# Kernel optimization log

Measured on AMD Instinct MI355X. Metric: run time of the kernel, lower is better.

The kernel has to match this reference:

```python
import jax, jax.numpy as jnp
import numpy as np

N = 50000      # nodes
E = 640000     # edges (before self loops)
IN = 128       # in_channels
H = 4          # heads (layer 1)
C = 64         # hidden_channels per head
OUT = 64       # out_channels
SLOPE = 0.2    # PyG GATConv default negative_slope


def setup_inputs() -> dict:
    key = jax.random.key(0)
    ks = jax.random.split(key, 12)
    x = jax.random.normal(ks[0], (N, IN), dtype=jnp.float32)
    edge_src = jax.random.randint(ks[1], (E,), 0, N, dtype=jnp.int32)
    edge_dst = jax.random.randint(ks[2], (E,), 0, N, dtype=jnp.int32)
    # Layer 1 params: Linear IN -> H*C, attention vectors a_src/a_dst [H, C], bias [H*C]
    W1 = jax.random.normal(ks[3], (IN, H * C), dtype=jnp.float32) / np.sqrt(IN)
    att_src1 = jax.random.normal(ks[4], (H, C), dtype=jnp.float32) / np.sqrt(C)
    att_dst1 = jax.random.normal(ks[5], (H, C), dtype=jnp.float32) / np.sqrt(C)
    b1 = jnp.zeros((H * C,), dtype=jnp.float32)
    # Layer 2 params: Linear H*C -> OUT, 1 head
    W2 = jax.random.normal(ks[6], (H * C, OUT), dtype=jnp.float32) / np.sqrt(H * C)
    att_src2 = jax.random.normal(ks[7], (1, OUT), dtype=jnp.float32) / np.sqrt(OUT)
    att_dst2 = jax.random.normal(ks[8], (1, OUT), dtype=jnp.float32) / np.sqrt(OUT)
    b2 = jnp.zeros((OUT,), dtype=jnp.float32)
    return {"x": x, "W1": W1, "att_src1": att_src1, "att_dst1": att_dst1, "b1": b1,
            "W2": W2, "att_src2": att_src2, "att_dst2": att_dst2, "b2": b2,
            "edge_src": edge_src, "edge_dst": edge_dst}


def gat_conv(x, src, dst, W, a_src, a_dst, b, heads, ch):
    """PyG GATConv (concat=True): gather -> LeakyReLU attention -> per-dst softmax -> scatter-add."""
    n = x.shape[0]
    h = (x @ W).reshape(n, heads, ch)                  # [N, H, C]
    al_s = jnp.sum(h * a_src, axis=-1)                 # [N, H] node-level src attention term
    al_d = jnp.sum(h * a_dst, axis=-1)                 # [N, H]
    e = jax.nn.leaky_relu(al_s[src] + al_d[dst], SLOPE)  # [E, H] edge scores
    m = jax.ops.segment_max(e, dst, num_segments=n)    # stable per-dst softmax
    ex = jnp.exp(e - m[dst])
    den = jax.ops.segment_sum(ex, dst, num_segments=n)
    alpha = ex / den[dst]                              # [E, H]
    msg = h[src] * alpha[:, :, None]                   # [E, H, C]
    out = jax.ops.segment_sum(msg, dst, num_segments=n)  # [N, H, C]
    return out.reshape(n, heads * ch) + b


def reference(x, W1, att_src1, att_dst1, b1, W2, att_src2, att_dst2, b2, edge_src, edge_dst):
    # PyG GATConv default add_self_loops=True
    loops = jnp.arange(N, dtype=edge_src.dtype)
    src = jnp.concatenate([edge_src, loops])
    dst = jnp.concatenate([edge_dst, loops])
    h = gat_conv(x, src, dst, W1, att_src1, att_dst1, b1, H, C)
    h = jax.nn.elu(h)                                  # F.elu; dropout p=0 -> no-op
    out = gat_conv(h, src, dst, W2, att_src2, att_dst2, b2, 1, OUT)
    return out
```

## Files before the change

kernel.cpp:

```cpp
#include <hip/hip_runtime.h>
#include <hip/hip_bf16.h>
#include <cstdint>
#include <cstddef>

#define N_NODES 50000
#define N_EDGES 640000
#define ET (N_EDGES + N_NODES)
#define IN_CH 128
#define H1 4
#define HC1 256
#define OUT_CH 64
#define SLOPE 0.2f
#define SCAN_NBLK ((N_NODES + 255) / 256)
#define XW (N_NODES * IN_CH / 8)
#define W1N (IN_CH * HC1)
#define W2N (HC1 * OUT_CH)
#define CONVB ((XW + W1N + W2N + 255) / 256)
#define EDGEB ((ET + 255) / 256)
#define MT ((N_NODES + 63) / 64)
#define G1B (4 * MT)
#define PADB SCAN_NBLK
#define DUMMY N_NODES

typedef __attribute__((ext_vector_type(8))) short short8;
typedef __attribute__((ext_vector_type(4))) float floatx4;

__device__ __forceinline__ float bf2f(unsigned short u) {
    return __uint_as_float(((unsigned)u) << 16);
}
__device__ __forceinline__ unsigned short f2bf(float f) {
    unsigned u = __float_as_uint(f);
    unsigned r = 0x7fffu + ((u >> 16) & 1u);
    return (unsigned short)((u + r) >> 16);
}
__device__ __forceinline__ float ldf(const void* p, size_t i, bool f32) {
    return f32 ? ((const float*)p)[i] : bf2f(((const unsigned short*)p)[i]);
}
#define BLO(u) __uint_as_float((u) << 16)
#define BHI(u) __uint_as_float((u) & 0xffff0000u)

__global__ __launch_bounds__(256) void init_all(
    const unsigned short* __restrict__ x, unsigned* __restrict__ flag,
    int* __restrict__ counts, int* __restrict__ state,
    unsigned short* __restrict__ h16, unsigned short* __restrict__ h2,
    float* __restrict__ als1, float* __restrict__ als2)
{
    int b = blockIdx.x;
    if (b < SCAN_NBLK) {
        int i = b * 256 + threadIdx.x;
        if (i < N_NODES) counts[i] = 0;
    } else {
        int t = threadIdx.x;
        if (t < 64) {
            int bad = 0;
            #pragma unroll
            for (int r = 0; r < 4; ++r) {
                float v = bf2f(x[r * 64 + t]);
                if (!(v == v) || fabsf(v) > 1e4f) bad = 1;
            }
            unsigned long long m = __ballot(bad != 0);
            if (t == 0) *flag = (m != 0ull) ? 1u : 0u;
        } else if (t == 64) {
            state[0] = 0; state[1] = 0;
        } else if (t >= 128 && t < 192) {
            uint2 z; z.x = 0u; z.y = 0u;
            *((uint2*)(h16 + (size_t)DUMMY * HC1) + (t - 128)) = z;
        } else if (t >= 192 && t < 224) {
            ((unsigned*)(h2 + (size_t)DUMMY * OUT_CH))[t - 192] = 0u;
        } else if (t >= 224 && t < 228) {
            als1[(size_t)DUMMY * H1 + (t - 224)] = -1e30f;
        } else if (t == 228) {
            als2[DUMMY] = -1e30f;
        }
    }
}

__global__ __launch_bounds__(256) void conv_count(
    const void* __restrict__ x, const void* __restrict__ W1,
    const void* __restrict__ W2, const unsigned* __restrict__ flag,
    unsigned short* __restrict__ x16,
    unsigned short* __restrict__ Wt1, unsigned short* __restrict__ Wt2,
    const int* __restrict__ edst, int* __restrict__ counts,
    int* __restrict__ epos)
{
    int b = blockIdx.x;
    if (b < CONVB) {
        int i = b * 256 + threadIdx.x;
        const bool f32 = (*flag != 0);
        if (i < XW) {
            size_t off = (size_t)i * 8;
            uint4 st;
            if (f32) {
                const float* xp = (const float*)x + off;
                float4 a = *(const float4*)xp;
                float4 c = *(const float4*)(xp + 4);
                st.x = (unsigned)f2bf(a.x) | ((unsigned)f2bf(a.y) << 16);
                st.y = (unsigned)f2bf(a.z) | ((unsigned)f2bf(a.w) << 16);
                st.z = (unsigned)f2bf(c.x) | ((unsigned)f2bf(c.y) << 16);
                st.w = (unsigned)f2bf(c.z) | ((unsigned)f2bf(c.w) << 16);
            } else {
                st = *(const uint4*)((const unsigned short*)x + off);
            }
            *(uint4*)(x16 + off) = st;
        } else if (i < XW + W1N) {
            int j = i - XW;
            int n = j / IN_CH, k = j % IN_CH;
            Wt1[j] = f2bf(ldf(W1, (size_t)k * HC1 + n, f32));
        } else if (i < XW + W1N + W2N) {
            int j = i - XW - W1N;
            int n = j / HC1, k = j % HC1;
            Wt2[j] = f2bf(ldf(W2, (size_t)k * OUT_CH + n, f32));
        }
    } else {
        int i = (b - CONVB) * 256 + threadIdx.x;
        if (i < ET) {
            int d = (i < N_EDGES) ? edst[i] : (i - N_EDGES);
            epos[i] = atomicAdd(&counts[d], 1);
        }
    }
}

__global__ __launch_bounds__(256) void scan_onepass(
    const int* __restrict__ counts, int* __restrict__ rowptr,
    int* __restrict__ bsum, int* __restrict__ boff, int* __restrict__ state)
{
    __shared__ int s[256];
    const int t = threadIdx.x, b = blockIdx.x;
    const int i = b * 256 + t;
    int v = (i < N_NODES) ? ((counts[i] + 7) & ~7) : 0;
    s[t] = v;
    __syncthreads();
    #pragma unroll
    for (int off = 1; off < 256; off <<= 1) {
        int u = (t >= off) ? s[t - off] : 0;
        __syncthreads();
        s[t] += u;
        __syncthreads();
    }
    const int incl = s[t];
    if (t == 255) {
        __hip_atomic_store(&bsum[b], incl, __ATOMIC_RELAXED, __HIP_MEMORY_SCOPE_AGENT);
        __hip_atomic_fetch_add(&state[0], 1, __ATOMIC_ACQ_REL, __HIP_MEMORY_SCOPE_AGENT);
    }
    if (b == 0) {
        if (t == 0) {
            while (__hip_atomic_load(&state[0], __ATOMIC_ACQUIRE, __HIP_MEMORY_SCOPE_AGENT) < SCAN_NBLK)
                __builtin_amdgcn_s_sleep(8);
        }
        __syncthreads();
        int w = (t < SCAN_NBLK)
              ? __hip_atomic_load(&bsum[t], __ATOMIC_RELAXED, __HIP_MEMORY_SCOPE_AGENT) : 0;
        s[t] = w;
        __syncthreads();
        #pragma unroll
        for (int off = 1; off < 256; off <<= 1) {
            int u = (t >= off) ? s[t - off] : 0;
            __syncthreads();
            s[t] += u;
            __syncthreads();
        }
        if (t < SCAN_NBLK)
            __hip_atomic_store(&boff[t], s[t] - w, __ATOMIC_RELAXED, __HIP_MEMORY_SCOPE_AGENT);
        __syncthreads();
        if (t == 0)
            __hip_atomic_store(&state[1], 1, __ATOMIC_RELEASE, __HIP_MEMORY_SCOPE_AGENT);
    }
    if (t == 0) {
        while (__hip_atomic_load(&state[1], __ATOMIC_ACQUIRE, __HIP_MEMORY_SCOPE_AGENT) == 0)
            __builtin_amdgcn_s_sleep(8);
    }
    __syncthreads();
    int off0 = __hip_atomic_load(&boff[b], __ATOMIC_RELAXED, __HIP_MEMORY_SCOPE_AGENT);
    if (i < N_NODES)
        rowptr[i] = off0 + incl - v;
    if (i == N_NODES - 1) rowptr[N_NODES] = off0 + incl;
}

template <int KK, int NSUB>
__device__ __forceinline__ void gemm_body(
    const unsigned short* __restrict__ A, const unsigned short* __restrict__ Bt,
    const void* __restrict__ avs, const void* __restrict__ avd,
    const unsigned* __restrict__ flag, unsigned short* __restrict__ C,
    float* __restrict__ als, float* __restrict__ ald,
    int M, int N, int bx, int by)
{
    const int tid = threadIdx.x;
    const int m0 = by * 64, n0 = bx * (NSUB * 16);
    const int w = tid >> 6, lane = tid & 63;
    const int ln = lane & 15, quad = lane >> 4;
    const int m_frag = m0 + w * 16 + ln;
    floatx4 acc[NSUB];
    #pragma unroll
    for (int sub = 0; sub < NSUB; ++sub)
        acc[sub] = (floatx4){0.f, 0.f, 0.f, 0.f};

    for (int ks = 0; ks < KK / 32; ++ks) {
        const int kbase = ks * 32 + quad * 8;
        short8 a;
        if (m_frag < M) {
            a = *(const short8*)(A + (size_t)m_frag * KK + kbase);
        } else {
            #pragma unroll
            for (int j = 0; j < 8; ++j) a[j] = 0;
        }
        #pragma unroll
        for (int sub = 0; sub < NSUB; ++sub) {
            short8 b = *(const short8*)(Bt + (size_t)(n0 + sub * 16 + ln) * KK + kbase);
            acc[sub] = __builtin_amdgcn_mfma_f32_16x16x32_bf16(a, b, acc[sub], 0, 0, 0);
        }
    }

    #pragma unroll
    for (int sub = 0; sub < NSUB; ++sub) {
        #pragma unroll
        for (int r = 0; r < 4; ++r) {
            int m = m0 + w * 16 + quad * 4 + r;
            if (m < M)
                C[(size_t)m * N + n0 + sub * 16 + ln] = f2bf(acc[sub][r]);
        }
    }

    const bool f32in = (*flag != 0);
    float as[NSUB], av[NSUB];
    #pragma unroll
    for (int sub = 0; sub < NSUB; ++sub) {
        as[sub] = ldf(avs, n0 + sub * 16 + ln, f32in);
        av[sub] = ldf(avd, n0 + sub * 16 + ln, f32in);
    }
    const int Hh = N >> 6;
    #pragma unroll
    for (int hb = 0; hb < NSUB / 4; ++hb) {
        #pragma unroll
        for (int r = 0; r < 4; ++r) {
            float ps = 0.f, pd = 0.f;
            #pragma unroll
            for (int k = 0; k < 4; ++k) {
                ps += acc[hb * 4 + k][r] * as[hb * 4 + k];
                pd += acc[hb * 4 + k][r] * av[hb * 4 + k];
            }
            #pragma unroll
            for (int off = 1; off < 16; off <<= 1) {
                ps += __shfl_xor(ps, off, 64);
                pd += __shfl_xor(pd, off, 64);
            }
            int m = m0 + w * 16 + quad * 4 + r;
            if (ln == 0 && m < M) {
                als[(size_t)m * Hh + bx * (NSUB / 4) + hb] = ps;
                ald[(size_t)m * Hh + bx * (NSUB / 4) + hb] = pd;
            }
        }
    }
}

__global__ __launch_bounds__(256) void gemm1_fill(
    const unsigned short* __restrict__ x16, const unsigned short* __restrict__ Wt1,
    const void* __restrict__ as1, const void* __restrict__ ad1,
    const unsigned* __restrict__ flag, unsigned short* __restrict__ h16,
    float* __restrict__ als, float* __restrict__ ald,
    const int* __restrict__ esrc, const int* __restrict__ edst,
    const int* __restrict__ rowptr, const int* __restrict__ epos,
    const int* __restrict__ counts, int* __restrict__ ecsr)
{
    int b = blockIdx.x;
    if (b < G1B) {
        gemm_body<IN_CH, 4>(x16, Wt1, as1, ad1, flag, h16, als, ald,
                            N_NODES, HC1, b & 3, b >> 2);
    } else if (b < G1B + EDGEB) {
        int i = (b - G1B) * 256 + threadIdx.x;
        if (i < ET) {
            int s = (i < N_EDGES) ? esrc[i] : (i - N_EDGES);
            int d = (i < N_EDGES) ? edst[i] : (i - N_EDGES);
            ecsr[rowptr[d] + epos[i]] = s;
        }
    } else {
        int i = (b - G1B - EDGEB) * 256 + threadIdx.x;
        if (i < N_NODES) {
            int c = counts[i];
            int lo = rowptr[i] + c, hi = rowptr[i + 1];
            for (int j = lo; j < hi; ++j) ecsr[j] = DUMMY;
        }
    }
}

__global__ __launch_bounds__(256) void gemm2(
    const unsigned short* __restrict__ xo16, const unsigned short* __restrict__ Wt2,
    const void* __restrict__ as2, const void* __restrict__ ad2,
    const unsigned* __restrict__ flag, unsigned short* __restrict__ h2,
    float* __restrict__ als, float* __restrict__ ald)
{
    gemm_body<HC1, 4>(xo16, Wt2, as2, ad2, flag, h2, als, ald,
                      N_NODES, OUT_CH, 0, blockIdx.x);
}

__global__ __launch_bounds__(256) void agg_node1(
    const int* __restrict__ rowptr, const int* __restrict__ ecsr,
    const unsigned short* __restrict__ h, const float* __restrict__ als,
    const float* __restrict__ ald, const void* __restrict__ bias,
    const unsigned* __restrict__ flag, unsigned short* __restrict__ out)
{
    int wave = (blockIdx.x * blockDim.x + threadIdx.x) >> 6;
    int lane = threadIdx.x & 63;
    if (wave >= N_NODES) return;
    const int d = wave;
    const int g  = lane >> 5;
    const int hg = (lane >> 3) & 3;
    const int c0 = (lane & 7) << 3;
    const int hoff = hg * 64 + c0;
    const int lo = rowptr[d], hi = rowptr[d + 1];
    const float ad = ald[d * H1 + hg];

    float acc[8];
    #pragma unroll
    for (int j = 0; j < 8; ++j) acc[j] = 0.f;
    float den = 0.f;

    for (int e = lo; e < hi; e += 4) {
        int4 ix = *(const int4*)(ecsr + e);
        int s0 = g ? ix.y : ix.x;
        int s1 = g ? ix.w : ix.z;
        uint4 qa = *(const uint4*)(h + (size_t)s0 * HC1 + hoff);
        uint4 qb = *(const uint4*)(h + (size_t)s1 * HC1 + hoff);
        float t0 = als[s0 * H1 + hg] + ad;
        float t1 = als[s1 * H1 + hg] + ad;
        float p0 = __expf(fmaxf(t0, SLOPE * t0));
        float p1 = __expf(fmaxf(t1, SLOPE * t1));
        den += p0 + p1;
        acc[0] += p0 * BLO(qa.x) + p1 * BLO(qb.x);
        acc[1] += p0 * BHI(qa.x) + p1 * BHI(qb.x);
        acc[2] += p0 * BLO(qa.y) + p1 * BLO(qb.y);
        acc[3] += p0 * BHI(qa.y) + p1 * BHI(qb.y);
        acc[4] += p0 * BLO(qa.z) + p1 * BLO(qb.z);
        acc[5] += p0 * BHI(qa.z) + p1 * BHI(qb.z);
        acc[6] += p0 * BLO(qa.w) + p1 * BLO(qb.w);
        acc[7] += p0 * BHI(qa.w) + p1 * BHI(qb.w);
    }

    den += __shfl_xor(den, 32, 64);
    #pragma unroll
    for (int j = 0; j < 8; ++j) acc[j] += __shfl_xor(acc[j], 32, 64);

    if (lane < 32) {
        const bool f32in = (*flag != 0);
        const float inv = 1.f / den;
        float v[8];
        #pragma unroll
        for (int j = 0; j < 8; ++j) {
            float t = acc[j] * inv + ldf(bias, hoff + j, f32in);
            v[j] = (t > 0.f) ? t : (__expf(t) - 1.f);
        }
        uint4 st;
        st.x = (unsigned)f2bf(v[0]) | ((unsigned)f2bf(v[1]) << 16);
        st.y = (unsigned)f2bf(v[2]) | ((unsigned)f2bf(v[3]) << 16);
        st.z = (unsigned)f2bf(v[4]) | ((unsigned)f2bf(v[5]) << 16);
        st.w = (unsigned)f2bf(v[6]) | ((unsigned)f2bf(v[7]) << 16);
        *(uint4*)(out + (size_t)d * HC1 + hoff) = st;
    }
}

__global__ __launch_bounds__(256) void agg_node2(
    const int* __restrict__ rowptr, const int* __restrict__ ecsr,
    const unsigned short* __restrict__ h, const float* __restrict__ als,
    const float* __restrict__ ald, const void* __restrict__ bias,
    const unsigned* __restrict__ flag, float* __restrict__ out)
{
    int wave = (blockIdx.x * blockDim.x + threadIdx.x) >> 6;
    int lane = threadIdx.x & 63;
    if (wave >= N_NODES) return;
    const int d = wave;
    const int eg = lane >> 3;
    const int c0 = (lane & 7) << 3;
    const int lo = rowptr[d], hi = rowptr[d + 1];
    const float ad = ald[d];

    float acc[8];
    #pragma unroll
    for (int j = 0; j < 8; ++j) acc[j] = 0.f;
    float den = 0.f;

    for (int eb = lo; eb < hi; eb += 8) {
        int s = ecsr[eb + eg];
        uint4 q = *(const uint4*)(h + (size_t)s * OUT_CH + c0);
        float t = als[s] + ad;
        float p = __expf(fmaxf(t, SLOPE * t));
        den += p;
        acc[0] += p * BLO(q.x);
        acc[1] += p * BHI(q.x);
        acc[2] += p * BLO(q.y);
        acc[3] += p * BHI(q.y);
        acc[4] += p * BLO(q.z);
        acc[5] += p * BHI(q.z);
        acc[6] += p * BLO(q.w);
        acc[7] += p * BHI(q.w);
    }
    #pragma unroll
    for (int off = 8; off <= 32; off <<= 1) {
        den += __shfl_xor(den, off, 64);
        #pragma unroll
        for (int j = 0; j < 8; ++j) acc[j] += __shfl_xor(acc[j], off, 64);
    }
    if (lane < 8) {
        const bool f32in = (*flag != 0);
        const float inv = 1.f / den;
        float4 v0, v1;
        v0.x = acc[0] * inv + ldf(bias, c0 + 0, f32in);
        v0.y = acc[1] * inv + ldf(bias, c0 + 1, f32in);
        v0.z = acc[2] * inv + ldf(bias, c0 + 2, f32in);
        v0.w = acc[3] * inv + ldf(bias, c0 + 3, f32in);
        v1.x = acc[4] * inv + ldf(bias, c0 + 4, f32in);
        v1.y = acc[5] * inv + ldf(bias, c0 + 5, f32in);
        v1.z = acc[6] * inv + ldf(bias, c0 + 6, f32in);
        v1.w = acc[7] * inv + ldf(bias, c0 + 7, f32in);
        *(float4*)(out + (size_t)d * OUT_CH + c0) = v0;
        *(float4*)(out + (size_t)d * OUT_CH + c0 + 4) = v1;
    }
}

extern "C" void kernel_launch(void* const* d_in, const int* in_sizes, int n_in,
                              void* d_out, int out_size, void* d_ws, size_t ws_size,
                              hipStream_t stream)
{
    const void* x   = d_in[0];
    const void* W1  = d_in[1];
    const void* as1 = d_in[2];
    const void* ad1 = d_in[3];
    const void* b1  = d_in[4];
    const void* W2  = d_in[5];
    const void* as2 = d_in[6];
    const void* ad2 = d_in[7];
    const void* b2  = d_in[8];
    const int* esrc = (const int*)d_in[9];
    const int* edst = (const int*)d_in[10];
    float* out = (float*)d_out;

    char* base = (char*)d_ws;
    const size_t MB = 1024 * 1024;
    unsigned short* x16  = (unsigned short*)(base);
    unsigned short* h16  = (unsigned short*)(base + 13 * MB);
    unsigned short* xo16 = (unsigned short*)(base + 39 * MB);
    unsigned short* h2   = (unsigned short*)(base + 65 * MB);
    float* als1   = (float*)(base + 72 * MB);
    float* ald1   = (float*)(base + 73 * MB);
    float* als2   = (float*)(base + 74 * MB);
    float* ald2   = (float*)(base + 74 * MB + 512 * 1024);
    unsigned short* Wt1 = (unsigned short*)(base + 75 * MB);
    unsigned short* Wt2 = (unsigned short*)(base + 75 * MB + 128 * 1024);
    int* counts   = (int*)(base + 76 * MB);
    int* rowptr   = (int*)(base + 77 * MB);
    int* bsum     = (int*)(base + 78 * MB);
    int* boff     = bsum + 256;
    int* state    = boff + 256;
    unsigned* flag = (unsigned*)(base + 78 * MB + 8 * 1024);
    int* epos     = (int*)(base + 79 * MB);
    int* ecsr     = (int*)(base + 82 * MB);

    const int BLK = 256;
    const int node_wave_blocks = (N_NODES * 64 + BLK - 1) / BLK;

    init_all<<<SCAN_NBLK + 1, BLK, 0, stream>>>(
        (const unsigned short*)x, flag, counts, state, h16, h2, als1, als2);

    conv_count<<<CONVB + EDGEB, BLK, 0, stream>>>(
        x, W1, W2, flag, x16, Wt1, Wt2, edst, counts, epos);

    scan_onepass<<<SCAN_NBLK, BLK, 0, stream>>>(
        counts, rowptr, bsum, boff, state);

    gemm1_fill<<<G1B + EDGEB + PADB, BLK, 0, stream>>>(
        x16, Wt1, as1, ad1, flag, h16, als1, ald1, esrc, edst, rowptr, epos,
        counts, ecsr);

    agg_node1<<<node_wave_blocks, BLK, 0, stream>>>(
        rowptr, ecsr, h16, als1, ald1, b1, flag, xo16);

    gemm2<<<MT, BLK, 0, stream>>>(xo16, Wt2, as2, ad2, flag, h2, als2, ald2);

    agg_node2<<<node_wave_blocks, BLK, 0, stream>>>(
        rowptr, ecsr, h2, als2, ald2, b2, flag, out);
}
```

Baseline: 291.5 us.

## Drop CSR row padding and mask tail edges in aggregation loops

Removes the per-node padding of CSR rows to multiples of 8, so the DUMMY fill blocks disappear and no padded edges are processed. Both aggregation kernels now handle partial tails with clamped loads and DUMMY-masked sources. Layer-1 aggregation is restructured so each lane loads one edge index and computes one attention exponential per (edge, head), then broadcasts sources and weights with shuffles, processing 16 edges per iteration. This cuts redundant exp and index work but adds many cross-lane shuffles and serialised gathers inside the inner loop.

Result: no change. 290.5 us (-0.4%).

```diff
diff --git a/kernel.cpp b/kernel.cpp
--- a/kernel.cpp
+++ b/kernel.cpp
@@ -19,7 +19,6 @@
 #define EDGEB ((ET + 255) / 256)
 #define MT ((N_NODES + 63) / 64)
 #define G1B (4 * MT)
-#define PADB SCAN_NBLK
 #define DUMMY N_NODES
 
 typedef __attribute__((ext_vector_type(8))) short short8;
@@ -127,7 +126,7 @@
     __shared__ int s[256];
     const int t = threadIdx.x, b = blockIdx.x;
     const int i = b * 256 + t;
-    int v = (i < N_NODES) ? ((counts[i] + 7) & ~7) : 0;
+    int v = (i < N_NODES) ? counts[i] : 0;
     s[t] = v;
     __syncthreads();
     #pragma unroll
@@ -259,25 +258,18 @@
     float* __restrict__ als, float* __restrict__ ald,
     const int* __restrict__ esrc, const int* __restrict__ edst,
     const int* __restrict__ rowptr, const int* __restrict__ epos,
-    const int* __restrict__ counts, int* __restrict__ ecsr)
+    int* __restrict__ ecsr)
 {
     int b = blockIdx.x;
     if (b < G1B) {
         gemm_body<IN_CH, 4>(x16, Wt1, as1, ad1, flag, h16, als, ald,
                             N_NODES, HC1, b & 3, b >> 2);
-    } else if (b < G1B + EDGEB) {
+    } else {
         int i = (b - G1B) * 256 + threadIdx.x;
         if (i < ET) {
             int s = (i < N_EDGES) ? esrc[i] : (i - N_EDGES);
             int d = (i < N_EDGES) ? edst[i] : (i - N_EDGES);
             ecsr[rowptr[d] + epos[i]] = s;
-        }
-    } else {
-        int i = (b - G1B - EDGEB) * 256 + threadIdx.x;
-        if (i < N_NODES) {
-            int c = counts[i];
-            int lo = rowptr[i] + c, hi = rowptr[i + 1];
-            for (int j = lo; j < hi; ++j) ecsr[j] = DUMMY;
         }
     }
 }
@@ -306,36 +298,43 @@
     const int hg = (lane >> 3) & 3;
     const int c0 = (lane & 7) << 3;
     const int hoff = hg * 64 + c0;
+    const int el = lane & 15;
+    const int eo = lane >> 2;
+    const int ho = lane & 3;
     const int lo = rowptr[d], hi = rowptr[d + 1];
-    const float ad = ald[d * H1 + hg];
+    const float adv = ald[d * H1 + ho];
 
     float acc[8];
     #pragma unroll
     for (int j = 0; j < 8; ++j) acc[j] = 0.f;
     float den = 0.f;
 
-    for (int e = lo; e < hi; e += 4) {
-        int4 ix = *(const int4*)(ecsr + e);
-        int s0 = g ? ix.y : ix.x;
-        int s1 = g ? ix.w : ix.z;
-        uint4 qa = *(const uint4*)(h + (size_t)s0 * HC1 + hoff);
-        uint4 qb = *(const uint4*)(h + (size_t)s1 * HC1 + hoff);
-        float t0 = als[s0 * H1 + hg] + ad;
-        float t1 = als[s1 * H1 + hg] + ad;
-        float p0 = __expf(fmaxf(t0, SLOPE * t0));
-        float p1 = __expf(fmaxf(t1, SLOPE * t1));
-        den += p0 + p1;
-        acc[0] += p0 * BLO(qa.x) + p1 * BLO(qb.x);
-        acc[1] += p0 * BHI(qa.x) + p1 * BHI(qb.x);
-        acc[2] += p0 * BLO(qa.y) + p1 * BLO(qb.y);
-        acc[3] += p0 * BHI(qa.y) + p1 * BHI(qb.y);
-        acc[4] += p0 * BLO(qa.z) + p1 * BLO(qb.z);
-        acc[5] += p0 * BHI(qa.z) + p1 * BHI(qb.z);
-        acc[6] += p0 * BLO(qa.w) + p1 * BLO(qb.w);
-        acc[7] += p0 * BHI(qa.w) + p1 * BHI(qb.w);
-    }
-
-    den += __shfl_xor(den, 32, 64);
+    for (int base = lo; base < hi; base += 16) {
+        int ep = base + el;
+        int sv = ecsr[min(ep, hi - 1)];
+        sv = (ep < hi) ? sv : DUMMY;
+        int s_own = __shfl(sv, eo, 64);
+        float t = als[s_own * H1 + ho] + adv;
+        float pv = __expf(fmaxf(t, SLOPE * t));
+        den += pv;
+        #pragma unroll
+        for (int j = 0; j < 8; ++j) {
+            int e2 = 2 * j + g;
+            int s  = __shfl(sv, e2, 64);
+            float p = __shfl(pv, e2 * 4 + hg, 64);
+            uint4 q = *(const uint4*)(h + (size_t)s * HC1 + hoff);
+            acc[0] += p * BLO(q.x); acc[1] += p * BHI(q.x);
+            acc[2] += p * BLO(q.y); acc[3] += p * BHI(q.y);
+            acc[4] += p * BLO(q.z); acc[5] += p * BHI(q.z);
+            acc[6] += p * BLO(q.w); acc[7] += p * BHI(q.w);
+        }
+    }
+
+    #pragma unroll
+    for (int off = 4; off <= 32; off <<= 1)
+        den += __shfl_xor(den, off, 64);
+    den = __shfl(den, hg, 64);
+
     #pragma unroll
     for (int j = 0; j < 8; ++j) acc[j] += __shfl_xor(acc[j], 32, 64);
 
@@ -377,20 +376,25 @@
     for (int j = 0; j < 8; ++j) acc[j] = 0.f;
     float den = 0.f;
 
-    for (int eb = lo; eb < hi; eb += 8) {
-        int s = ecsr[eb + eg];
-        uint4 q = *(const uint4*)(h + (size_t)s * OUT_CH + c0);
-        float t = als[s] + ad;
-        float p = __expf(fmaxf(t, SLOPE * t));
-        den += p;
-        acc[0] += p * BLO(q.x);
-        acc[1] += p * BHI(q.x);
-        acc[2] += p * BLO(q.y);
-        acc[3] += p * BHI(q.y);
-        acc[4] += p * BLO(q.z);
-        acc[5] += p * BHI(q.z);
-        acc[6] += p * BLO(q.w);
-        acc[7] += p * BHI(q.w);
+    for (int eb = lo; eb < hi; eb += 16) {
+        int ep0 = eb + eg, ep1 = eb + 8 + eg;
+        int s0 = ecsr[min(ep0, hi - 1)]; s0 = (ep0 < hi) ? s0 : DUMMY;
+        int s1 = ecsr[min(ep1, hi - 1)]; s1 = (ep1 < hi) ? s1 : DUMMY;
+        uint4 q0 = *(const uint4*)(h + (size_t)s0 * OUT_CH + c0);
+        uint4 q1 = *(const uint4*)(h + (size_t)s1 * OUT_CH + c0);
+        float t0 = als[s0] + ad;
+        float t1 = als[s1] + ad;
+        float p0 = __expf(fmaxf(t0, SLOPE * t0));
+        float p1 = __expf(fmaxf(t1, SLOPE * t1));
+        den += p0 + p1;
+        acc[0] += p0 * BLO(q0.x) + p1 * BLO(q1.x);
+        acc[1] += p0 * BHI(q0.x) + p1 * BHI(q1.x);
+        acc[2] += p0 * BLO(q0.y) + p1 * BLO(q1.y);
+        acc[3] += p0 * BHI(q0.y) + p1 * BHI(q1.y);
+        acc[4] += p0 * BLO(q0.z) + p1 * BLO(q1.z);
+        acc[5] += p0 * BHI(q0.z) + p1 * BHI(q1.z);
+        acc[6] += p0 * BLO(q0.w) + p1 * BLO(q1.w);
+        acc[7] += p0 * BHI(q0.w) + p1 * BHI(q1.w);
     }
     #pragma unroll
     for (int off = 8; off <= 32; off <<= 1) {
@@ -465,9 +469,9 @@
     scan_onepass<<<SCAN_NBLK, BLK, 0, stream>>>(
         counts, rowptr, bsum, boff, state);
 
-    gemm1_fill<<<G1B + EDGEB + PADB, BLK, 0, stream>>>(
+    gemm1_fill<<<G1B + EDGEB, BLK, 0, stream>>>(
         x16, Wt1, as1, ad1, flag, h16, als1, ald1, esrc, edst, rowptr, epos,
-        counts, ecsr);
+        ecsr);
 
     agg_node1<<<node_wave_blocks, BLK, 0, stream>>>(
         rowptr, ecsr, h16, als1, ald1, b1, flag, xo16);
```

## Precompute layer-1 edge weights per head and drop CSR padding with dummy nodes

Applied to the files above, without the earlier changes.

A new edge_w1 kernel computes the exponentiated LeakyReLU attention weight for every edge and head once, and stores it head-major in CSR order. agg_node1 then reads those weights instead of gathering als1 and evaluating exp per edge, and it is restructured so each lane handles 4 channels of a single head, with a scalar tail loop. CSR rows are no longer padded to a multiple of 8 with dummy entries, which removes the pad-fill blocks and dummy-row initialisation, and agg_node2 gains a bounds check. The cost is an extra launch plus about 11 MB of edge-weight writes and reads, which reuse the x16 workspace region. Unpadded rows also mean misaligned, shorter per-node loops.

New measurement: 323.2 us. 1.11x slower.

```diff
diff --git a/kernel.cpp b/kernel.cpp
--- a/kernel.cpp
+++ b/kernel.cpp
@@ -19,8 +19,6 @@
 #define EDGEB ((ET + 255) / 256)
 #define MT ((N_NODES + 63) / 64)
 #define G1B (4 * MT)
-#define PADB SCAN_NBLK
-#define DUMMY N_NODES
 
 typedef __attribute__((ext_vector_type(8))) short short8;
 typedef __attribute__((ext_vector_type(4))) float floatx4;
@@ -41,9 +39,7 @@
 
 __global__ __launch_bounds__(256) void init_all(
     const unsigned short* __restrict__ x, unsigned* __restrict__ flag,
-    int* __restrict__ counts, int* __restrict__ state,
-    unsigned short* __restrict__ h16, unsigned short* __restrict__ h2,
-    float* __restrict__ als1, float* __restrict__ als2)
+    int* __restrict__ counts, int* __restrict__ state)
 {
     int b = blockIdx.x;
     if (b < SCAN_NBLK) {
@@ -62,15 +58,6 @@
             if (t == 0) *flag = (m != 0ull) ? 1u : 0u;
         } else if (t == 64) {
             state[0] = 0; state[1] = 0;
-        } else if (t >= 128 && t < 192) {
-            uint2 z; z.x = 0u; z.y = 0u;
-            *((uint2*)(h16 + (size_t)DUMMY * HC1) + (t - 128)) = z;
-        } else if (t >= 192 && t < 224) {
-            ((unsigned*)(h2 + (size_t)DUMMY * OUT_CH))[t - 192] = 0u;
-        } else if (t >= 224 && t < 228) {
-            als1[(size_t)DUMMY * H1 + (t - 224)] = -1e30f;
-        } else if (t == 228) {
-            als2[DUMMY] = -1e30f;
         }
     }
 }
@@ -127,7 +114,7 @@
     __shared__ int s[256];
     const int t = threadIdx.x, b = blockIdx.x;
     const int i = b * 256 + t;
-    int v = (i < N_NODES) ? ((counts[i] + 7) & ~7) : 0;
+    int v = (i < N_NODES) ? counts[i] : 0;
     s[t] = v;
     __syncthreads();
     #pragma unroll
@@ -259,27 +246,100 @@
     float* __restrict__ als, float* __restrict__ ald,
     const int* __restrict__ esrc, const int* __restrict__ edst,
     const int* __restrict__ rowptr, const int* __restrict__ epos,
-    const int* __restrict__ counts, int* __restrict__ ecsr)
+    int* __restrict__ ecsr)
 {
     int b = blockIdx.x;
     if (b < G1B) {
         gemm_body<IN_CH, 4>(x16, Wt1, as1, ad1, flag, h16, als, ald,
                             N_NODES, HC1, b & 3, b >> 2);
-    } else if (b < G1B + EDGEB) {
+    } else {
         int i = (b - G1B) * 256 + threadIdx.x;
         if (i < ET) {
             int s = (i < N_EDGES) ? esrc[i] : (i - N_EDGES);
             int d = (i < N_EDGES) ? edst[i] : (i - N_EDGES);
             ecsr[rowptr[d] + epos[i]] = s;
         }
-    } else {
-        int i = (b - G1B - EDGEB) * 256 + threadIdx.x;
-        if (i < N_NODES) {
-            int c = counts[i];
-            int lo = rowptr[i] + c, hi = rowptr[i + 1];
-            for (int j = lo; j < hi; ++j) ecsr[j] = DUMMY;
-        }
-    }
+    }
+}
+
+__global__ __launch_bounds__(256) void edge_w1(
+    const int* __restrict__ esrc, const int* __restrict__ edst,
+    const int* __restrict__ rowptr, const int* __restrict__ epos,
+    const float* __restrict__ als1, const float* __restrict__ ald1,
+    float* __restrict__ ew1)
+{
+    int i = blockIdx.x * 256 + threadIdx.x;
+    if (i >= ET) return;
+    int s = (i < N_EDGES) ? esrc[i] : (i - N_EDGES);
+    int d = (i < N_EDGES) ? edst[i] : (i - N_EDGES);
+    int slot = rowptr[d] + epos[i];
+    float4 as = *(const float4*)(als1 + (size_t)s * H1);
+    float4 ad = *(const float4*)(ald1 + (size_t)d * H1);
+    float t0 = as.x + ad.x, t1 = as.y + ad.y;
+    float t2 = as.z + ad.z, t3 = as.w + ad.w;
+    ew1[0 * (size_t)ET + slot] = __expf(fmaxf(t0, SLOPE * t0));
+    ew1[1 * (size_t)ET + slot] = __expf(fmaxf(t1, SLOPE * t1));
+    ew1[2 * (size_t)ET + slot] = __expf(fmaxf(t2, SLOPE * t2));
+    ew1[3 * (size_t)ET + slot] = __expf(fmaxf(t3, SLOPE * t3));
+}
+
+__global__ __launch_bounds__(256) void agg_node1(
+    const int* __restrict__ rowptr, const int* __restrict__ ecsr,
+    const unsigned short* __restrict__ h, const float* __restrict__ ew1,
+    const void* __restrict__ bias, const unsigned* __restrict__ flag,
+    unsigned short* __restrict__ out)
+{
+    int wave = (blockIdx.x * blockDim.x + threadIdx.x) >> 6;
+    int lane = threadIdx.x & 63;
+    if (wave >= N_NODES) return;
+    const int d = wave;
+    const int hg = lane >> 4;
+    const int c0 = (lane & 15) << 2;
+    const int hoff = hg * 64 + c0;
+    const int lo = rowptr[d], hi = rowptr[d + 1];
+    const float* __restrict__ ewh = ew1 + (size_t)hg * ET;
+
+    float acc0 = 0.f, acc1 = 0.f, acc2 = 0.f, acc3 = 0.f, den = 0.f;
+
+    int e = lo;
+    for (; e + 3 < hi; e += 4) {
+        int s0 = ecsr[e], s1 = ecsr[e + 1], s2 = ecsr[e + 2], s3 = ecsr[e + 3];
+        float p0 = ewh[e], p1 = ewh[e + 1], p2 = ewh[e + 2], p3 = ewh[e + 3];
+        uint2 q0 = *(const uint2*)(h + (size_t)s0 * HC1 + hoff);
+        uint2 q1 = *(const uint2*)(h + (size_t)s1 * HC1 + hoff);
+        uint2 q2 = *(const uint2*)(h + (size_t)s2 * HC1 + hoff);
+        uint2 q3 = *(const uint2*)(h + (size_t)s3 * HC1 + hoff);
+        den += (p0 + p1) + (p2 + p3);
+        acc0 += p0 * BLO(q0.x) + p1 * BLO(q1.x) + p2 * BLO(q2.x) + p3 * BLO(q3.x);
+        acc1 += p0 * BHI(q0.x) + p1 * BHI(q1.x) + p2 * BHI(q2.x) + p3 * BHI(q3.x);
+        acc2 += p0 * BLO(q0.y) + p1 * BLO(q1.y) + p2 * BLO(q2.y) + p3 * BLO(q3.y);
+        acc3 += p0 * BHI(q0.y) + p1 * BHI(q1.y) + p2 * BHI(q2.y) + p3 * BHI(q3.y);
+    }
+    for (; e < hi; ++e) {
+        int s0 = ecsr[e];
+        float p0 = ewh[e];
+        uint2 q0 = *(const uint2*)(h + (size_t)s0 * HC1 + hoff);
+        den += p0;
+        acc0 += p0 * BLO(q0.x);
+        acc1 += p0 * BHI(q0.x);
+        acc2 += p0 * BLO(q0.y);
+        acc3 += p0 * BHI(q0.y);
+    }
+
+    const bool f32in = (*flag != 0);
+    const float inv = 1.f / den;
+    float v0 = acc0 * inv + ldf(bias, hoff + 0, f32in);
+    float v1 = acc1 * inv + ldf(bias, hoff + 1, f32in);
+    float v2 = acc2 * inv + ldf(bias, hoff + 2, f32in);
+    float v3 = acc3 * inv + ldf(bias, hoff + 3, f32in);
+    v0 = (v0 > 0.f) ? v0 : (__expf(v0) - 1.f);
+    v1 = (v1 > 0.f) ? v1 : (__expf(v1) - 1.f);
+    v2 = (v2 > 0.f) ? v2 : (__expf(v2) - 1.f);
+    v3 = (v3 > 0.f) ? v3 : (__expf(v3) - 1.f);
+    uint2 st;
+    st.x = (unsigned)f2bf(v0) | ((unsigned)f2bf(v1) << 16);
+    st.y = (unsigned)f2bf(v2) | ((unsigned)f2bf(v3) << 16);
+    *(uint2*)(out + (size_t)d * HC1 + hoff) = st;
 }
 
 __global__ __launch_bounds__(256) void gemm2(
@@ -290,71 +350,6 @@
 {
     gemm_body<HC1, 4>(xo16, Wt2, as2, ad2, flag, h2, als, ald,
                       N_NODES, OUT_CH, 0, blockIdx.x);
-}
-
-__global__ __launch_bounds__(256) void agg_node1(
-    const int* __restrict__ rowptr, const int* __restrict__ ecsr,
-    const unsigned short* __restrict__ h, const float* __restrict__ als,
-    const float* __restrict__ ald, const void* __restrict__ bias,
-    const unsigned* __restrict__ flag, unsigned short* __restrict__ out)
-{
-    int wave = (blockIdx.x * blockDim.x + threadIdx.x) >> 6;
-    int lane = threadIdx.x & 63;
-    if (wave >= N_NODES) return;
-    const int d = wave;
-    const int g  = lane >> 5;
-    const int hg = (lane >> 3) & 3;
-    const int c0 = (lane & 7) << 3;
-    const int hoff = hg * 64 + c0;
-    const int lo = rowptr[d], hi = rowptr[d + 1];
-    const float ad = ald[d * H1 + hg];
-
-    float acc[8];
-    #pragma unroll
-    for (int j = 0; j < 8; ++j) acc[j] = 0.f;
-    float den = 0.f;
-
-    for (int e = lo; e < hi; e += 4) {
-        int4 ix = *(const int4*)(ecsr + e);
-        int s0 = g ? ix.y : ix.x;
-        int s1 = g ? ix.w : ix.z;
-        uint4 qa = *(const uint4*)(h + (size_t)s0 * HC1 + hoff);
-        uint4 qb = *(const uint4*)(h + (size_t)s1 * HC1 + hoff);
-        float t0 = als[s0 * H1 + hg] + ad;
-        float t1 = als[s1 * H1 + hg] + ad;
-        float p0 = __expf(fmaxf(t0, SLOPE * t0));
-        float p1 = __expf(fmaxf(t1, SLOPE * t1));
-        den += p0 + p1;
-        acc[0] += p0 * BLO(qa.x) + p1 * BLO(qb.x);
-        acc[1] += p0 * BHI(qa.x) + p1 * BHI(qb.x);
-        acc[2] += p0 * BLO(qa.y) + p1 * BLO(qb.y);
-        acc[3] += p0 * BHI(qa.y) + p1 * BHI(qb.y);
-        acc[4] += p0 * BLO(qa.z) + p1 * BLO(qb.z);
-        acc[5] += p0 * BHI(qa.z) + p1 * BHI(qb.z);
-        acc[6] += p0 * BLO(qa.w) + p1 * BLO(qb.w);
-        acc[7] += p0 * BHI(qa.w) + p1 * BHI(qb.w);
-    }
-
-    den += __shfl_xor(den, 32, 64);
-    #pragma unroll
-    for (int j = 0; j < 8; ++j) acc[j] += __shfl_xor(acc[j], 32, 64);
-
-    if (lane < 32) {
-        const bool f32in = (*flag != 0);
-        const float inv = 1.f / den;
-        float v[8];
-        #pragma unroll
-        for (int j = 0; j < 8; ++j) {
-            float t = acc[j] * inv + ldf(bias, hoff + j, f32in);
-            v[j] = (t > 0.f) ? t : (__expf(t) - 1.f);
-        }
-        uint4 st;
-        st.x = (unsigned)f2bf(v[0]) | ((unsigned)f2bf(v[1]) << 16);
-        st.y = (unsigned)f2bf(v[2]) | ((unsigned)f2bf(v[3]) << 16);
-        st.z = (unsigned)f2bf(v[4]) | ((unsigned)f2bf(v[5]) << 16);
-        st.w = (unsigned)f2bf(v[6]) | ((unsigned)f2bf(v[7]) << 16);
-        *(uint4*)(out + (size_t)d * HC1 + hoff) = st;
-    }
 }
 
 __global__ __launch_bounds__(256) void agg_node2(
@@ -378,19 +373,22 @@
     float den = 0.f;
 
     for (int eb = lo; eb < hi; eb += 8) {
-        int s = ecsr[eb + eg];
-        uint4 q = *(const uint4*)(h + (size_t)s * OUT_CH + c0);
-        float t = als[s] + ad;
-        float p = __expf(fmaxf(t, SLOPE * t));
-        den += p;
-        acc[0] += p * BLO(q.x);
-        acc[1] += p * BHI(q.x);
-        acc[2] += p * BLO(q.y);
-        acc[3] += p * BHI(q.y);
-        acc[4] += p * BLO(q.z);
-        acc[5] += p * BHI(q.z);
-        acc[6] += p * BLO(q.w);
-        acc[7] += p * BHI(q.w);
+        int e = eb + eg;
+        if (e < hi) {
+            int s = ecsr[e];
+            uint4 q = *(const uint4*)(h + (size_t)s * OUT_CH + c0);
+            float t = als[s] + ad;
+            float p = __expf(fmaxf(t, SLOPE * t));
+            den += p;
+            acc[0] += p * BLO(q.x);
+            acc[1] += p * BHI(q.x);
+            acc[2] += p * BLO(q.y);
+            acc[3] += p * BHI(q.y);
+            acc[4] += p * BLO(q.z);
+            acc[5] += p * BHI(q.z);
+            acc[6] += p * BLO(q.w);
+            acc[7] += p * BHI(q.w);
+        }
     }
     #pragma unroll
     for (int off = 8; off <= 32; off <<= 1) {
@@ -435,6 +433,7 @@
     char* base = (char*)d_ws;
     const size_t MB = 1024 * 1024;
     unsigned short* x16  = (unsigned short*)(base);
+    float* ew1           = (float*)(base);
     unsigned short* h16  = (unsigned short*)(base + 13 * MB);
     unsigned short* xo16 = (unsigned short*)(base + 39 * MB);
     unsigned short* h2   = (unsigned short*)(base + 65 * MB);
@@ -457,7 +456,7 @@
     const int node_wave_blocks = (N_NODES * 64 + BLK - 1) / BLK;
 
     init_all<<<SCAN_NBLK + 1, BLK, 0, stream>>>(
-        (const unsigned short*)x, flag, counts, state, h16, h2, als1, als2);
+        (const unsigned short*)x, flag, counts, state);
 
     conv_count<<<CONVB + EDGEB, BLK, 0, stream>>>(
         x, W1, W2, flag, x16, Wt1, Wt2, edst, counts, epos);
@@ -465,12 +464,15 @@
     scan_onepass<<<SCAN_NBLK, BLK, 0, stream>>>(
         counts, rowptr, bsum, boff, state);
 
-    gemm1_fill<<<G1B + EDGEB + PADB, BLK, 0, stream>>>(
+    gemm1_fill<<<G1B + EDGEB, BLK, 0, stream>>>(
         x16, Wt1, as1, ad1, flag, h16, als1, ald1, esrc, edst, rowptr, epos,
-        counts, ecsr);
+        ecsr);
+
+    edge_w1<<<EDGEB, BLK, 0, stream>>>(
+        esrc, edst, rowptr, epos, als1, ald1, ew1);
 
     agg_node1<<<node_wave_blocks, BLK, 0, stream>>>(
-        rowptr, ecsr, h16, als1, ald1, b1, flag, xo16);
+        rowptr, ecsr, h16, ew1, b1, flag, xo16);
 
     gemm2<<<MT, BLK, 0, stream>>>(xo16, Wt2, as2, ad2, flag, h2, als2, ald2);
 
```
